# Optimization experiments

Measured on AMD Instinct MI355X. Metric: run time of the kernel, lower is better.

Reference implementation:

```python
import jax, jax.numpy as jnp
import numpy as np

T, D, H, F, A = 65536, 128, 128, 100, 18  # steps, obs_dim, gru hidden, head width, n_actions


def setup_inputs() -> dict:
    key = jax.random.key(0)
    ks = jax.random.split(key, 20)
    p = lambda k, shape, s=0.05: jax.random.normal(k, shape, dtype=jnp.float32) * s
    return {
        "obs": jax.random.normal(ks[0], (T, D), dtype=jnp.float32),
        "W1": p(ks[1], (D, H)), "b1": jnp.zeros((H,), jnp.float32),
        # GRU layer 1: gates kernel [x;h]->2H, candidate kernel [x;r*h]->H
        "Wg1": p(ks[2], (H + H, 2 * H)), "bg1": jnp.zeros((2 * H,), jnp.float32),
        "Wc1": p(ks[3], (H + H, H)), "bc1": jnp.zeros((H,), jnp.float32),
        # GRU layer 2
        "Wg2": p(ks[4], (H + H, 2 * H)), "bg2": jnp.zeros((2 * H,), jnp.float32),
        "Wc2": p(ks[5], (H + H, H)), "bc2": jnp.zeros((H,), jnp.float32),
        "W2": p(ks[6], (H, F)), "b2": jnp.zeros((F,), jnp.float32),
        "W3": p(ks[7], (H, F)), "b3": jnp.zeros((F,), jnp.float32),
        "Wp": p(ks[8], (F, A), 0.01), "bp": jnp.zeros((A,), jnp.float32),
        "Wv": p(ks[9], (F, 1)), "bv": jnp.zeros((1,), jnp.float32),
    }


def _gru_step(h, x, Wg, bg, Wc, bc):
    # TF GRUCell math: r,u = sigmoid([x;h]Wg + bg); c = tanh([x; r*h]Wc + bc)
    g = jax.nn.sigmoid(jnp.concatenate([x, h], -1) @ Wg + bg)
    r, u = jnp.split(g, 2, axis=-1)
    c = jnp.tanh(jnp.concatenate([x, r * h], -1) @ Wc + bc)
    return u * h + (1.0 - u) * c


def reference(obs, W1, b1, Wg1, bg1, Wc1, bc1, Wg2, bg2, Wc2, bc2,
              W2, b2, W3, b3, Wp, bp, Wv, bv):
    x = jax.nn.relu(obs @ W1 + b1)  # [T, H]

    def step(carry, xt):
        h1, h2 = carry
        h1 = _gru_step(h1, xt, Wg1, bg1, Wc1, bc1)
        h2 = _gru_step(h2, h1, Wg2, bg2, Wc2, bc2)
        return (h1, h2), h2

    h0 = (jnp.zeros((H,), x.dtype), jnp.zeros((H,), x.dtype))  # zero_state, batch=1
    (h1, h2), ys = jax.lax.scan(step, h0, x)  # ys: [T, H]

    pi = jax.nn.relu(ys @ W2 + b2)
    v = jax.nn.relu(ys @ W3 + b3)
    logits = pi @ Wp + bp   # [T, A]
    value = v @ Wv + bv     # [T, 1]
    return logits, value, h1, h2
```

## Files before the change

kernel.cpp:

```cpp
#include <hip/hip_runtime.h>

#define T_STEPS 65536
#define SCHUNK 128
#define NCHUNK 512
#define RING 8


typedef float f2 __attribute__((ext_vector_type(2)));
typedef float f4 __attribute__((ext_vector_type(4)));

__device__ __forceinline__ float sigmoid_f(float x) {
  float e = __expf(-x);
  return __builtin_amdgcn_rcpf(1.0f + e);
}
__device__ __forceinline__ float tanh_f(float x) {
  float e = __expf(-2.0f * x);
  return (1.0f - e) * __builtin_amdgcn_rcpf(1.0f + e);
}

__device__ __forceinline__ void bar_lds() {
  asm volatile("s_waitcnt lgkmcnt(0)\n\ts_barrier" ::: "memory");
}

__device__ __forceinline__ float rdlane(float v, int lane) {
  return __int_as_float(__builtin_amdgcn_readlane(__float_as_int(v), lane));
}

__device__ __forceinline__ void spin_rlx(int* p) {
  while (__hip_atomic_load(p, __ATOMIC_RELAXED, __HIP_MEMORY_SCOPE_AGENT) == 0)
    __builtin_amdgcn_s_sleep(8);
}
__device__ __forceinline__ void spin_acq(int* p) {
  spin_rlx(p);
  (void)__hip_atomic_load(p, __ATOMIC_ACQUIRE, __HIP_MEMORY_SCOPE_AGENT);
}
__device__ __forceinline__ void set_flag_rel(int* p) {
  __hip_atomic_store(p, 1, __ATOMIC_RELEASE, __HIP_MEMORY_SCOPE_AGENT);
}
__device__ __forceinline__ void set_flag_rlx(int* p) {
  __hip_atomic_store(p, 1, __ATOMIC_RELAXED, __HIP_MEMORY_SCOPE_AGENT);
}

__global__ __launch_bounds__(256)
void gemm_k128(const float* __restrict__ IN, const float* __restrict__ W,
               const float* __restrict__ bias, float* __restrict__ OUT,
               int N, int relu) {
  __shared__ __align__(16) float in_t[32][132];
  const int tid = threadIdx.x;
  const int ct = tid & 63;
  const int rt = tid >> 6;
  const int R0 = blockIdx.x * 32;

  const f4* src = (const f4*)(IN + (size_t)R0 * 128);
#pragma unroll
  for (int q = 0; q < 4; ++q) {
    int f4i = tid + 256 * q;
    int r = f4i >> 5, c4 = f4i & 31;
    f4 v = src[f4i];
    *(f4*)&in_t[r][c4 * 4] = v;
  }
  __syncthreads();

  f2 acc[8][4];
#pragma unroll
  for (int r = 0; r < 8; ++r)
#pragma unroll
    for (int m = 0; m < 4; ++m) acc[r][m] = (f2)0.0f;

  for (int kp = 0; kp < 64; ++kp) {
    f2 iv[8];
#pragma unroll
    for (int r = 0; r < 8; ++r)
      iv[r] = *(const f2*)&in_t[rt * 8 + r][2 * kp];
    f2 wv[4];
#pragma unroll
    for (int m = 0; m < 4; ++m) {
      int c = ct + 64 * m;
      if (c < N) {
        wv[m].x = W[(2 * kp) * N + c];
        wv[m].y = W[(2 * kp + 1) * N + c];
      } else {
        wv[m] = (f2)0.0f;
      }
    }
#pragma unroll
    for (int r = 0; r < 8; ++r)
#pragma unroll
      for (int m = 0; m < 4; ++m)
        acc[r][m] = __builtin_elementwise_fma(iv[r], wv[m], acc[r][m]);
  }

#pragma unroll
  for (int m = 0; m < 4; ++m) {
    int c = ct + 64 * m;
    if (c < N) {
      float b = bias[c];
#pragma unroll
      for (int r = 0; r < 8; ++r) {
        float v = acc[r][m].x + acc[r][m].y + b;
        if (relu) v = fmaxf(v, 0.0f);
        OUT[(size_t)(R0 + rt * 8 + r) * N + c] = v;
      }
    }
  }
}

#define GRU_STEP(LT, AR, AU, CXV)                                             \
  do {                                                                        \
    f2 ga0 = (f2)0.0f, ga1 = (f2)0.0f, ga2 = (f2)0.0f, ga3 = (f2)0.0f;        \
    _Pragma("unroll")                                                         \
    for (int qq = 0; qq < 16; ++qq) {                                         \
      f2 hp;                                                                  \
      hp.x = rdlane(hself, 2 * qq);                                           \
      hp.y = rdlane(hself, 2 * qq + 1);                                       \
      ga0 = __builtin_elementwise_fma(hp, wgt[qq][0], ga0);                   \
      ga1 = __builtin_elementwise_fma(hp, wgt[qq][1], ga1);                   \
      ga2 = __builtin_elementwise_fma(hp, wgt[qq][2], ga2);                   \
      ga3 = __builtin_elementwise_fma(hp, wgt[qq][3], ga3);                   \
    }                                                                         \
    pg[(l + 0) * 5 + w] = ga0.x + ga0.y;                                      \
    pg[(l + 64) * 5 + w] = ga1.x + ga1.y;                                     \
    pg[(l + 128) * 5 + w] = ga2.x + ga2.y;                                    \
    pg[(l + 192) * 5 + w] = ga3.x + ga3.y;                                    \
    bar_lds();                                                                \
    float rpre = ((pg[o_r * 5 + 0] + pg[o_r * 5 + 1]) +                       \
                  (pg[o_r * 5 + 2] + pg[o_r * 5 + 3])) + (AR);                \
    float upre = ((pg[o_u * 5 + 0] + pg[o_u * 5 + 1]) +                       \
                  (pg[o_u * 5 + 2] + pg[o_u * 5 + 3])) + (AU);                \
    float rg = sigmoid_f(rpre);                                               \
    float ugv = sigmoid_f(upre);                                              \
    float rhv = rg * hself;                                                   \
    f2 ca0 = (f2)0.0f, ca1 = (f2)0.0f;                                        \
    _Pragma("unroll")                                                         \
    for (int qq = 0; qq < 16; ++qq) {                                         \
      f2 rp;                                                                  \
      rp.x = rdlane(rhv, 2 * qq);                                             \
      rp.y = rdlane(rhv, 2 * qq + 1);                                         \
      ca0 = __builtin_elementwise_fma(rp, wct[qq][0], ca0);                   \
      ca1 = __builtin_elementwise_fma(rp, wct[qq][1], ca1);                   \
    }                                                                         \
    pc[(l + 0) * 5 + w] = ca0.x + ca0.y;                                      \
    pc[(l + 64) * 5 + w] = ca1.x + ca1.y;                                     \
    bar_lds();                                                                \
    float cpre = ((pc[o_r * 5 + 0] + pc[o_r * 5 + 1]) +                       \
                  (pc[o_r * 5 + 2] + pc[o_r * 5 + 3])) + (CXV);               \
    float cv = tanh_f(cpre);                                                  \
    hself = ugv * hself + (1.0f - ugv) * cv;                                  \
    if (half == 0) hc[(LT) * 128 + o_r] = hself;                              \
  } while (0)

__device__ void scan_role(const float* __restrict__ A, const float* __restrict__ CX,
                          const float* __restrict__ Wgh, const float* __restrict__ Wch,
                          float* __restrict__ hout, int hout_is_ring,
                          float* __restrict__ hfinal,
                          int* relf, int* acka, int* ackb, int* wfa, int* wfb) {
  __shared__ float pg[256 * 5];
  __shared__ float pc[128 * 5];
  const int tid = threadIdx.x;
  const int w = tid >> 6;
  const int l = tid & 63;
  const int j = l & 31;
  const int half = l >> 5;
  const int o_r = 32 * w + j;
  const int o_u = o_r + 128;

  f2 wgt[16][4];
  f2 wct[16][2];
#pragma unroll
  for (int q = 0; q < 16; ++q) {
#pragma unroll
    for (int m = 0; m < 4; ++m) {
      wgt[q][m].x = Wgh[(32 * w + 2 * q) * 256 + l + 64 * m];
      wgt[q][m].y = Wgh[(32 * w + 2 * q + 1) * 256 + l + 64 * m];
    }
#pragma unroll
    for (int n = 0; n < 2; ++n) {
      wct[q][n].x = Wch[(32 * w + 2 * q) * 128 + l + 64 * n];
      wct[q][n].y = Wch[(32 * w + 2 * q + 1) * 128 + l + 64 * n];
    }
  }

  float hself = 0.0f;

  for (int c = 0; c < NCHUNK; ++c) {
    if (wfa) { spin_acq(&wfa[c]); spin_acq(&wfb[c]); }
    if (relf && c >= RING) {
      spin_rlx(&acka[c - RING]);
      spin_rlx(&ackb[c - RING]);
    }
    const float* Ac = A + (size_t)c * SCHUNK * 256;
    const float* Cc = CX + (size_t)c * SCHUNK * 128;
    float* hc = hout_is_ring ? hout + (size_t)(c & (RING - 1)) * SCHUNK * 128
                             : hout + (size_t)c * SCHUNK * 128;

    float arc[4], auc[4], cxc[4], arn[4], aun[4], cxn[4];
#pragma unroll
    for (int q = 0; q < 4; ++q) {
      arc[q] = Ac[q * 256 + o_r];
      auc[q] = Ac[q * 256 + o_u];
      cxc[q] = Cc[q * 128 + o_r];
    }
    for (int t0 = 0; t0 < SCHUNK; t0 += 4) {
      const int nb = (t0 + 4 < SCHUNK) ? t0 + 4 : 0;
#pragma unroll
      for (int q = 0; q < 4; ++q) {
        arn[q] = Ac[(nb + q) * 256 + o_r];
        aun[q] = Ac[(nb + q) * 256 + o_u];
        cxn[q] = Cc[(nb + q) * 128 + o_r];
      }
#pragma unroll
      for (int q = 0; q < 4; ++q) {
        GRU_STEP(t0 + q, arc[q], auc[q], cxc[q]);
      }
#pragma unroll
      for (int q = 0; q < 4; ++q) { arc[q] = arn[q]; auc[q] = aun[q]; cxc[q] = cxn[q]; }
    }
    if (relf) {
      __syncthreads();
      if (tid == 0) set_flag_rel(&relf[c]);
    }
  }
  if (half == 0) hfinal[o_r] = hself;
}

__global__ void dummy_decl_anchor() {}

__device__ void gemv_gate_role(const float* __restrict__ ring,
                               const float* __restrict__ W,
                               const float* __restrict__ bias,
                               float* __restrict__ OUT,
                               int* inflag, int* ack, int* outflag) {
  __shared__ __align__(16) float hst[SCHUNK * 128];
  const int tid = threadIdx.x;
  const int l = tid & 63;
  const int col = tid;

  f2 wcol[64];
#pragma unroll
  for (int q = 0; q < 64; ++q) {
    wcol[q].x = W[(2 * q) * 256 + col];
    wcol[q].y = W[(2 * q + 1) * 256 + col];
  }
  const float bcol = bias[col];

  for (int c = 0; c < NCHUNK; ++c) {
    spin_acq(&inflag[c]);
    const f4* slot = (const f4*)(ring + (size_t)(c & (RING - 1)) * SCHUNK * 128);
    f4* hst4 = (f4*)hst;
#pragma unroll
    for (int q = 0; q < 16; ++q) hst4[tid + 256 * q] = slot[tid + 256 * q];
    __syncthreads();
    if (tid == 0) set_flag_rlx(&ack[c]);

    float* outc = OUT + (size_t)c * SCHUNK * 256;
    for (int t = 0; t < SCHUNK; ++t) {
      f2 hreg = *(const f2*)&hst[t * 128 + 2 * l];
      f2 a0 = (f2)0.0f, a1 = (f2)0.0f, a2 = (f2)0.0f, a3 = (f2)0.0f;
#pragma unroll
      for (int q = 0; q < 16; ++q) {
        f2 h0, h1, h2, h3;
        h0.x = rdlane(hreg.x, 4 * q);     h0.y = rdlane(hreg.y, 4 * q);
        h1.x = rdlane(hreg.x, 4 * q + 1); h1.y = rdlane(hreg.y, 4 * q + 1);
        h2.x = rdlane(hreg.x, 4 * q + 2); h2.y = rdlane(hreg.y, 4 * q + 2);
        h3.x = rdlane(hreg.x, 4 * q + 3); h3.y = rdlane(hreg.y, 4 * q + 3);
        a0 = __builtin_elementwise_fma(h0, wcol[4 * q], a0);
        a1 = __builtin_elementwise_fma(h1, wcol[4 * q + 1], a1);
        a2 = __builtin_elementwise_fma(h2, wcol[4 * q + 2], a2);
        a3 = __builtin_elementwise_fma(h3, wcol[4 * q + 3], a3);
      }
      f2 s = (a0 + a1) + (a2 + a3);
      outc[t * 256 + col] = s.x + s.y + bcol;
    }
    __syncthreads();
    if (tid == 0) set_flag_rel(&outflag[c]);
  }
}

__device__ void gemv_cand_role(const float* __restrict__ ring,
                               const float* __restrict__ W,
                               const float* __restrict__ bias,
                               float* __restrict__ OUT,
                               int* inflag, int* ack, int* outflag) {
  __shared__ __align__(16) float hst[SCHUNK * 128];
  const int tid = threadIdx.x;
  const int l = tid & 63;
  const int col = tid & 127;
  const int par = tid >> 7;

  f2 wcol[64];
#pragma unroll
  for (int q = 0; q < 64; ++q) {
    wcol[q].x = W[(2 * q) * 128 + col];
    wcol[q].y = W[(2 * q + 1) * 128 + col];
  }
  const float bcol = bias[col];

  for (int c = 0; c < NCHUNK; ++c) {
    spin_acq(&inflag[c]);
    const f4* slot = (const f4*)(ring + (size_t)(c & (RING - 1)) * SCHUNK * 128);
    f4* hst4 = (f4*)hst;
#pragma unroll
    for (int q = 0; q < 16; ++q) hst4[tid + 256 * q] = slot[tid + 256 * q];
    __syncthreads();
    if (tid == 0) set_flag_rlx(&ack[c]);

    float* outc = OUT + (size_t)c * SCHUNK * 128;
    for (int s = 0; s < SCHUNK / 2; ++s) {
      const int t = 2 * s + par;
      f2 hreg = *(const f2*)&hst[t * 128 + 2 * l];
      f2 a0 = (f2)0.0f, a1 = (f2)0.0f, a2 = (f2)0.0f, a3 = (f2)0.0f;
#pragma unroll
      for (int q = 0; q < 16; ++q) {
        f2 h0, h1, h2, h3;
        h0.x = rdlane(hreg.x, 4 * q);     h0.y = rdlane(hreg.y, 4 * q);
        h1.x = rdlane(hreg.x, 4 * q + 1); h1.y = rdlane(hreg.y, 4 * q + 1);
        h2.x = rdlane(hreg.x, 4 * q + 2); h2.y = rdlane(hreg.y, 4 * q + 2);
        h3.x = rdlane(hreg.x, 4 * q + 3); h3.y = rdlane(hreg.y, 4 * q + 3);
        a0 = __builtin_elementwise_fma(h0, wcol[4 * q], a0);
        a1 = __builtin_elementwise_fma(h1, wcol[4 * q + 1], a1);
        a2 = __builtin_elementwise_fma(h2, wcol[4 * q + 2], a2);
        a3 = __builtin_elementwise_fma(h3, wcol[4 * q + 3], a3);
      }
      f2 sm = (a0 + a1) + (a2 + a3);
      outc[t * 128 + col] = sm.x + sm.y + bcol;
    }
    __syncthreads();
    if (tid == 0) set_flag_rel(&outflag[c]);
  }
}

__global__ __launch_bounds__(256, 1)
void pipeline(const float* __restrict__ A1, const float* __restrict__ C1X,
              const float* __restrict__ Wg1, const float* __restrict__ Wc1,
              const float* __restrict__ Wg2, const float* __restrict__ bg2,
              const float* __restrict__ Wc2, const float* __restrict__ bc2,
              float* ring, float* A2, float* C2X, float* YS,
              float* h1f, float* h2f, int* flags) {
  int* flag1 = flags;
  int* acka  = flags + 512;
  int* ackb  = flags + 1024;
  int* f2a   = flags + 1536;
  int* f2b   = flags + 2048;
  const int role = blockIdx.x;
  if (role == 0)
    scan_role(A1, C1X, Wg1 + 128 * 256, Wc1 + 128 * 128, ring, 1, h1f,
              flag1, acka, ackb, nullptr, nullptr);
  else if (role == 1)
    gemv_gate_role(ring, Wg2, bg2, A2, flag1, acka, f2a);
  else if (role == 2)
    gemv_cand_role(ring, Wc2, bc2, C2X, flag1, ackb, f2b);
  else
    scan_role(A2, C2X, Wg2 + 128 * 256, Wc2 + 128 * 128, YS, 0, h2f,
              nullptr, nullptr, nullptr, f2a, f2b);
}

__global__ __launch_bounds__(256)
void proj_heads(const float* __restrict__ PI, const float* __restrict__ V,
                const float* __restrict__ Wp, const float* __restrict__ bp,
                const float* __restrict__ Wv, const float* __restrict__ bv,
                float* __restrict__ logits, float* __restrict__ value) {
  __shared__ float pi_t[128][101];
  __shared__ float v_t[128][101];
  __shared__ float wp_s[100][18];
  __shared__ float wv_s[100];
  __shared__ float bp_s[18];
  __shared__ float bv_s;
  const int tid = threadIdx.x;
  const int R0 = blockIdx.x * 128;

  for (int idx = tid; idx < 12800; idx += 256) {
    int r = idx / 100, c = idx - r * 100;
    pi_t[r][c] = PI[(size_t)R0 * 100 + idx];
    v_t[r][c] = V[(size_t)R0 * 100 + idx];
  }
  for (int idx = tid; idx < 1800; idx += 256) ((float*)wp_s)[idx] = Wp[idx];
  if (tid < 100) wv_s[tid] = Wv[tid];
  if (tid < 18) bp_s[tid] = bp[tid];
  if (tid == 0) bv_s = bv[0];
  __syncthreads();

  const int r = tid >> 1, h = tid & 1;
  float acc[9];
#pragma unroll
  for (int m = 0; m < 9; ++m) acc[m] = bp_s[h * 9 + m];
  float vacc = bv_s;
#pragma unroll 4
  for (int c = 0; c < 100; ++c) {
    float p = pi_t[r][c];
#pragma unroll
    for (int m = 0; m < 9; ++m) acc[m] = fmaf(p, wp_s[c][h * 9 + m], acc[m]);
    if (h) vacc = fmaf(v_t[r][c], wv_s[c], vacc);
  }
  size_t t = (size_t)R0 + r;
#pragma unroll
  for (int m = 0; m < 9; ++m) logits[t * 18 + h * 9 + m] = acc[m];
  if (h) value[t] = vacc;
}

extern "C" void kernel_launch(void* const* d_in, const int* in_sizes, int n_in,
                              void* d_out, int out_size, void* d_ws, size_t ws_size,
                              hipStream_t stream) {
  const float* obs = (const float*)d_in[0];
  const float* W1  = (const float*)d_in[1];
  const float* b1  = (const float*)d_in[2];
  const float* Wg1 = (const float*)d_in[3];
  const float* bg1 = (const float*)d_in[4];
  const float* Wc1 = (const float*)d_in[5];
  const float* bc1 = (const float*)d_in[6];
  const float* Wg2 = (const float*)d_in[7];
  const float* bg2 = (const float*)d_in[8];
  const float* Wc2 = (const float*)d_in[9];
  const float* bc2 = (const float*)d_in[10];
  const float* W2  = (const float*)d_in[11];
  const float* b2  = (const float*)d_in[12];
  const float* W3  = (const float*)d_in[13];
  const float* b3  = (const float*)d_in[14];
  const float* Wp  = (const float*)d_in[15];
  const float* bp  = (const float*)d_in[16];
  const float* Wv  = (const float*)d_in[17];
  const float* bv  = (const float*)d_in[18];

  float* out = (float*)d_out;
  float* ws  = (float*)d_ws;
  const int T = T_STEPS;

  float* A1   = ws + 0;
  float* C1X  = ws + 16777216;
  float* ring = ws + 25165824;
  int*   flags = (int*)(ws + 25296896);
  float* X    = ws + 33554432;
  float* YS   = ws + 33554432;
  float* PIb  = ws + 0;
  float* Vb   = ws + 8388608;

  float* logits = out;
  float* value  = out + (size_t)T * 18;
  float* h1f    = out + (size_t)T * 18 + T;
  float* h2f    = h1f + 128;

  dim3 b256(256);
  hipMemsetAsync(flags, 0, 2560 * sizeof(int), stream);
  gemm_k128<<<T / 32, b256, 0, stream>>>(obs, W1, b1, X, 128, 1);
  gemm_k128<<<T / 32, b256, 0, stream>>>(X, Wg1, bg1, A1, 256, 0);
  gemm_k128<<<T / 32, b256, 0, stream>>>(X, Wc1, bc1, C1X, 128, 0);
  pipeline<<<4, b256, 0, stream>>>(A1, C1X, Wg1, Wc1, Wg2, bg2, Wc2, bc2,
                                   ring, A1 , C1X , YS,
                                   h1f, h2f, flags);
  gemm_k128<<<T / 32, b256, 0, stream>>>(YS, W2, b2, PIb, 100, 1);
  gemm_k128<<<T / 32, b256, 0, stream>>>(YS, W3, b3, Vb, 100, 1);
  proj_heads<<<T / 128, b256, 0, stream>>>(PIb, Vb, Wp, bp, Wv, bv, logits, value);
}
```

Baseline: 53.06 ms.

## Double pipeline block width to 512 threads, splitting recurrent matvec across eight waves

The persistent pipeline kernel now launches with 512 threads per role block instead of 256. In the GRU scan roles, each of the eight waves handles 16 rows of the hidden-state reduction instead of 32, which halves the per-wave serial FMA/lane-read chain on the recurrence's critical path. The cost is an 8-way partial-sum reduction through LDS instead of a 4-way one. The GEMV roles split timesteps across the extra threads, and the LDS staging buffer moves into the kernel so the roles share one allocation. The risks are more barrier cost per step with eight waves and higher register pressure under the new launch bounds.

```diff
diff --git a/kernel.cpp b/kernel.cpp
--- a/kernel.cpp
+++ b/kernel.cpp
@@ -109,44 +109,50 @@
   do {                                                                        \
     f2 ga0 = (f2)0.0f, ga1 = (f2)0.0f, ga2 = (f2)0.0f, ga3 = (f2)0.0f;        \
     _Pragma("unroll")                                                         \
-    for (int qq = 0; qq < 16; ++qq) {                                         \
+    for (int m = 0; m < 8; ++m) {                                             \
       f2 hp;                                                                  \
-      hp.x = rdlane(hself, 2 * qq);                                           \
-      hp.y = rdlane(hself, 2 * qq + 1);                                       \
-      ga0 = __builtin_elementwise_fma(hp, wgt[qq][0], ga0);                   \
-      ga1 = __builtin_elementwise_fma(hp, wgt[qq][1], ga1);                   \
-      ga2 = __builtin_elementwise_fma(hp, wgt[qq][2], ga2);                   \
-      ga3 = __builtin_elementwise_fma(hp, wgt[qq][3], ga3);                   \
+      hp.x = rdlane(hself, 2 * m);                                            \
+      hp.y = rdlane(hself, 2 * m + 1);                                        \
+      ga0 = __builtin_elementwise_fma(hp, wgt[m][0], ga0);                    \
+      ga1 = __builtin_elementwise_fma(hp, wgt[m][1], ga1);                    \
+      ga2 = __builtin_elementwise_fma(hp, wgt[m][2], ga2);                    \
+      ga3 = __builtin_elementwise_fma(hp, wgt[m][3], ga3);                    \
     }                                                                         \
-    pg[(l + 0) * 5 + w] = ga0.x + ga0.y;                                      \
-    pg[(l + 64) * 5 + w] = ga1.x + ga1.y;                                     \
-    pg[(l + 128) * 5 + w] = ga2.x + ga2.y;                                    \
-    pg[(l + 192) * 5 + w] = ga3.x + ga3.y;                                    \
+    pg[(l + 0) * 9 + w] = ga0.x + ga0.y;                                      \
+    pg[(l + 64) * 9 + w] = ga1.x + ga1.y;                                     \
+    pg[(l + 128) * 9 + w] = ga2.x + ga2.y;                                    \
+    pg[(l + 192) * 9 + w] = ga3.x + ga3.y;                                    \
     bar_lds();                                                                \
-    float rpre = ((pg[o_r * 5 + 0] + pg[o_r * 5 + 1]) +                       \
-                  (pg[o_r * 5 + 2] + pg[o_r * 5 + 3])) + (AR);                \
-    float upre = ((pg[o_u * 5 + 0] + pg[o_u * 5 + 1]) +                       \
-                  (pg[o_u * 5 + 2] + pg[o_u * 5 + 3])) + (AU);                \
+    float rpre = (((pg[o_r * 9 + 0] + pg[o_r * 9 + 1]) +                      \
+                   (pg[o_r * 9 + 2] + pg[o_r * 9 + 3])) +                     \
+                  ((pg[o_r * 9 + 4] + pg[o_r * 9 + 5]) +                      \
+                   (pg[o_r * 9 + 6] + pg[o_r * 9 + 7]))) + (AR);              \
+    float upre = (((pg[o_u * 9 + 0] + pg[o_u * 9 + 1]) +                      \
+                   (pg[o_u * 9 + 2] + pg[o_u * 9 + 3])) +                     \
+                  ((pg[o_u * 9 + 4] + pg[o_u * 9 + 5]) +                      \
+                   (pg[o_u * 9 + 6] + pg[o_u * 9 + 7]))) + (AU);              \
     float rg = sigmoid_f(rpre);                                               \
     float ugv = sigmoid_f(upre);                                              \
     float rhv = rg * hself;                                                   \
     f2 ca0 = (f2)0.0f, ca1 = (f2)0.0f;                                        \
     _Pragma("unroll")                                                         \
-    for (int qq = 0; qq < 16; ++qq) {                                         \
+    for (int m = 0; m < 8; ++m) {                                             \
       f2 rp;                                                                  \
-      rp.x = rdlane(rhv, 2 * qq);                                             \
-      rp.y = rdlane(rhv, 2 * qq + 1);                                         \
-      ca0 = __builtin_elementwise_fma(rp, wct[qq][0], ca0);                   \
-      ca1 = __builtin_elementwise_fma(rp, wct[qq][1], ca1);                   \
+      rp.x = rdlane(rhv, 2 * m);                                              \
+      rp.y = rdlane(rhv, 2 * m + 1);                                          \
+      ca0 = __builtin_elementwise_fma(rp, wct[m][0], ca0);                    \
+      ca1 = __builtin_elementwise_fma(rp, wct[m][1], ca1);                    \
     }                                                                         \
-    pc[(l + 0) * 5 + w] = ca0.x + ca0.y;                                      \
-    pc[(l + 64) * 5 + w] = ca1.x + ca1.y;                                     \
+    pc[(l + 0) * 9 + w] = ca0.x + ca0.y;                                      \
+    pc[(l + 64) * 9 + w] = ca1.x + ca1.y;                                     \
     bar_lds();                                                                \
-    float cpre = ((pc[o_r * 5 + 0] + pc[o_r * 5 + 1]) +                       \
-                  (pc[o_r * 5 + 2] + pc[o_r * 5 + 3])) + (CXV);               \
+    float cpre = (((pc[o_r * 9 + 0] + pc[o_r * 9 + 1]) +                      \
+                   (pc[o_r * 9 + 2] + pc[o_r * 9 + 3])) +                     \
+                  ((pc[o_r * 9 + 4] + pc[o_r * 9 + 5]) +                      \
+                   (pc[o_r * 9 + 6] + pc[o_r * 9 + 7]))) + (CXV);             \
     float cv = tanh_f(cpre);                                                  \
     hself = ugv * hself + (1.0f - ugv) * cv;                                  \
-    if (half == 0) hc[(LT) * 128 + o_r] = hself;                              \
+    if (l < 16) hc[(LT) * 128 + o_r] = hself;                                 \
   } while (0)
 
 __device__ void scan_role(const float* __restrict__ A, const float* __restrict__ CX,
@@ -154,29 +160,28 @@
                           float* __restrict__ hout, int hout_is_ring,
                           float* __restrict__ hfinal,
                           int* relf, int* acka, int* ackb, int* wfa, int* wfb) {
-  __shared__ float pg[256 * 5];
-  __shared__ float pc[128 * 5];
+  __shared__ float pg[256 * 9];
+  __shared__ float pc[128 * 9];
   const int tid = threadIdx.x;
   const int w = tid >> 6;
   const int l = tid & 63;
-  const int j = l & 31;
-  const int half = l >> 5;
-  const int o_r = 32 * w + j;
+  const int j = l & 15;
+  const int o_r = 16 * w + j;
   const int o_u = o_r + 128;
 
-  f2 wgt[16][4];
-  f2 wct[16][2];
-#pragma unroll
-  for (int q = 0; q < 16; ++q) {
-#pragma unroll
-    for (int m = 0; m < 4; ++m) {
-      wgt[q][m].x = Wgh[(32 * w + 2 * q) * 256 + l + 64 * m];
-      wgt[q][m].y = Wgh[(32 * w + 2 * q + 1) * 256 + l + 64 * m];
-    }
-#pragma unroll
-    for (int n = 0; n < 2; ++n) {
-      wct[q][n].x = Wch[(32 * w + 2 * q) * 128 + l + 64 * n];
-      wct[q][n].y = Wch[(32 * w + 2 * q + 1) * 128 + l + 64 * n];
+  f2 wgt[8][4];
+  f2 wct[8][2];
+#pragma unroll
+  for (int m = 0; m < 8; ++m) {
+#pragma unroll
+    for (int c = 0; c < 4; ++c) {
+      wgt[m][c].x = Wgh[(16 * w + 2 * m) * 256 + l + 64 * c];
+      wgt[m][c].y = Wgh[(16 * w + 2 * m + 1) * 256 + l + 64 * c];
+    }
+#pragma unroll
+    for (int c = 0; c < 2; ++c) {
+      wct[m][c].x = Wch[(16 * w + 2 * m) * 128 + l + 64 * c];
+      wct[m][c].y = Wch[(16 * w + 2 * m + 1) * 128 + l + 64 * c];
     }
   }
 
@@ -220,20 +225,19 @@
       if (tid == 0) set_flag_rel(&relf[c]);
     }
   }
-  if (half == 0) hfinal[o_r] = hself;
-}
-
-__global__ void dummy_decl_anchor() {}
+  if (l < 16) hfinal[o_r] = hself;
+}
 
 __device__ void gemv_gate_role(const float* __restrict__ ring,
                                const float* __restrict__ W,
                                const float* __restrict__ bias,
                                float* __restrict__ OUT,
-                               int* inflag, int* ack, int* outflag) {
-  __shared__ __align__(16) float hst[SCHUNK * 128];
+                               int* inflag, int* ack, int* outflag,
+                               float* hst) {
   const int tid = threadIdx.x;
   const int l = tid & 63;
-  const int col = tid;
+  const int col = tid & 255;
+  const int par = tid >> 8;
 
   f2 wcol[64];
 #pragma unroll
@@ -248,12 +252,13 @@
     const f4* slot = (const f4*)(ring + (size_t)(c & (RING - 1)) * SCHUNK * 128);
     f4* hst4 = (f4*)hst;
 #pragma unroll
-    for (int q = 0; q < 16; ++q) hst4[tid + 256 * q] = slot[tid + 256 * q];
+    for (int q = 0; q < 8; ++q) hst4[tid + 512 * q] = slot[tid + 512 * q];
     __syncthreads();
     if (tid == 0) set_flag_rlx(&ack[c]);
 
     float* outc = OUT + (size_t)c * SCHUNK * 256;
-    for (int t = 0; t < SCHUNK; ++t) {
+    for (int s = 0; s < SCHUNK / 2; ++s) {
+      const int t = 2 * s + par;
       f2 hreg = *(const f2*)&hst[t * 128 + 2 * l];
       f2 a0 = (f2)0.0f, a1 = (f2)0.0f, a2 = (f2)0.0f, a3 = (f2)0.0f;
 #pragma unroll
@@ -268,8 +273,8 @@
         a2 = __builtin_elementwise_fma(h2, wcol[4 * q + 2], a2);
         a3 = __builtin_elementwise_fma(h3, wcol[4 * q + 3], a3);
       }
-      f2 s = (a0 + a1) + (a2 + a3);
-      outc[t * 256 + col] = s.x + s.y + bcol;
+      f2 sm = (a0 + a1) + (a2 + a3);
+      outc[t * 256 + col] = sm.x + sm.y + bcol;
     }
     __syncthreads();
     if (tid == 0) set_flag_rel(&outflag[c]);
@@ -280,8 +285,8 @@
                                const float* __restrict__ W,
                                const float* __restrict__ bias,
                                float* __restrict__ OUT,
-                               int* inflag, int* ack, int* outflag) {
-  __shared__ __align__(16) float hst[SCHUNK * 128];
+                               int* inflag, int* ack, int* outflag,
+                               float* hst) {
   const int tid = threadIdx.x;
   const int l = tid & 63;
   const int col = tid & 127;
@@ -300,13 +305,13 @@
     const f4* slot = (const f4*)(ring + (size_t)(c & (RING - 1)) * SCHUNK * 128);
     f4* hst4 = (f4*)hst;
 #pragma unroll
-    for (int q = 0; q < 16; ++q) hst4[tid + 256 * q] = slot[tid + 256 * q];
+    for (int q = 0; q < 8; ++q) hst4[tid + 512 * q] = slot[tid + 512 * q];
     __syncthreads();
     if (tid == 0) set_flag_rlx(&ack[c]);
 
     float* outc = OUT + (size_t)c * SCHUNK * 128;
-    for (int s = 0; s < SCHUNK / 2; ++s) {
-      const int t = 2 * s + par;
+    for (int s = 0; s < SCHUNK / 4; ++s) {
+      const int t = 4 * s + par;
       f2 hreg = *(const f2*)&hst[t * 128 + 2 * l];
       f2 a0 = (f2)0.0f, a1 = (f2)0.0f, a2 = (f2)0.0f, a3 = (f2)0.0f;
 #pragma unroll
@@ -329,13 +334,14 @@
   }
 }
 
-__global__ __launch_bounds__(256, 1)
+__global__ __launch_bounds__(512, 2)
 void pipeline(const float* __restrict__ A1, const float* __restrict__ C1X,
               const float* __restrict__ Wg1, const float* __restrict__ Wc1,
               const float* __restrict__ Wg2, const float* __restrict__ bg2,
               const float* __restrict__ Wc2, const float* __restrict__ bc2,
               float* ring, float* A2, float* C2X, float* YS,
               float* h1f, float* h2f, int* flags) {
+  __shared__ __align__(16) float hst[SCHUNK * 128];
   int* flag1 = flags;
   int* acka  = flags + 512;
   int* ackb  = flags + 1024;
@@ -346,9 +352,9 @@
     scan_role(A1, C1X, Wg1 + 128 * 256, Wc1 + 128 * 128, ring, 1, h1f,
               flag1, acka, ackb, nullptr, nullptr);
   else if (role == 1)
-    gemv_gate_role(ring, Wg2, bg2, A2, flag1, acka, f2a);
+    gemv_gate_role(ring, Wg2, bg2, A2, flag1, acka, f2a, hst);
   else if (role == 2)
-    gemv_cand_role(ring, Wc2, bc2, C2X, flag1, ackb, f2b);
+    gemv_cand_role(ring, Wc2, bc2, C2X, flag1, ackb, f2b, hst);
   else
     scan_role(A2, C2X, Wg2 + 128 * 256, Wc2 + 128 * 128, YS, 0, h2f,
               nullptr, nullptr, nullptr, f2a, f2b);
@@ -443,9 +449,9 @@
   gemm_k128<<<T / 32, b256, 0, stream>>>(obs, W1, b1, X, 128, 1);
   gemm_k128<<<T / 32, b256, 0, stream>>>(X, Wg1, bg1, A1, 256, 0);
   gemm_k128<<<T / 32, b256, 0, stream>>>(X, Wc1, bc1, C1X, 128, 0);
-  pipeline<<<4, b256, 0, stream>>>(A1, C1X, Wg1, Wc1, Wg2, bg2, Wc2, bc2,
-                                   ring, A1 , C1X , YS,
-                                   h1f, h2f, flags);
+  pipeline<<<4, dim3(512), 0, stream>>>(A1, C1X, Wg1, Wc1, Wg2, bg2, Wc2, bc2,
+                                        ring, A1 , C1X , YS,
+                                        h1f, h2f, flags);
   gemm_k128<<<T / 32, b256, 0, stream>>>(YS, W2, b2, PIb, 100, 1);
   gemm_k128<<<T / 32, b256, 0, stream>>>(YS, W3, b3, Vb, 100, 1);
   proj_heads<<<T / 128, b256, 0, stream>>>(PIb, Vb, Wp, bp, Wv, bv, logits, value);
```

Result: slower. 56.86 ms (+7.2%).

## Merge both GRU layer scans into one 512-thread block with a chunk lag

Applied to the files above, without the earlier changes.

Layer-1 and layer-2 recurrent scans now run as two wave groups inside a single 512-thread block, with layer 2 trailing by two chunks. Both groups share the per-step barriers, and an `act` predicate masks out the inactive group during the prologue and epilogue. The gate and candidate GEMV roles also move to 512 threads, split the timesteps across thread halves, and use one shared LDS staging buffer, so the pipeline drops from 4 blocks to 3. The aim is to use more threads per block and fewer blocks. The cost is that the two scans are coupled in lockstep and compete for the same CU's SIMDs, which may lengthen the serial critical path.

```diff
diff --git a/kernel.cpp b/kernel.cpp
--- a/kernel.cpp
+++ b/kernel.cpp
@@ -4,6 +4,7 @@
 #define SCHUNK 128
 #define NCHUNK 512
 #define RING 8
+#define LAG 2
 
 
 typedef float f2 __attribute__((ext_vector_type(2)));
@@ -107,62 +108,79 @@
 
 #define GRU_STEP(LT, AR, AU, CXV)                                             \
   do {                                                                        \
-    f2 ga0 = (f2)0.0f, ga1 = (f2)0.0f, ga2 = (f2)0.0f, ga3 = (f2)0.0f;        \
-    _Pragma("unroll")                                                         \
-    for (int qq = 0; qq < 16; ++qq) {                                         \
-      f2 hp;                                                                  \
-      hp.x = rdlane(hself, 2 * qq);                                           \
-      hp.y = rdlane(hself, 2 * qq + 1);                                       \
-      ga0 = __builtin_elementwise_fma(hp, wgt[qq][0], ga0);                   \
-      ga1 = __builtin_elementwise_fma(hp, wgt[qq][1], ga1);                   \
-      ga2 = __builtin_elementwise_fma(hp, wgt[qq][2], ga2);                   \
-      ga3 = __builtin_elementwise_fma(hp, wgt[qq][3], ga3);                   \
+    if (act) {                                                                \
+      f2 ga0 = (f2)0.0f, ga1 = (f2)0.0f, ga2 = (f2)0.0f, ga3 = (f2)0.0f;      \
+      _Pragma("unroll")                                                       \
+      for (int qq = 0; qq < 16; ++qq) {                                       \
+        f2 hp;                                                                \
+        hp.x = rdlane(hself, 2 * qq);                                         \
+        hp.y = rdlane(hself, 2 * qq + 1);                                     \
+        ga0 = __builtin_elementwise_fma(hp, wgt[qq][0], ga0);                 \
+        ga1 = __builtin_elementwise_fma(hp, wgt[qq][1], ga1);                 \
+        ga2 = __builtin_elementwise_fma(hp, wgt[qq][2], ga2);                 \
+        ga3 = __builtin_elementwise_fma(hp, wgt[qq][3], ga3);                 \
+      }                                                                       \
+      pg[(l + 0) * 5 + w] = ga0.x + ga0.y;                                    \
+      pg[(l + 64) * 5 + w] = ga1.x + ga1.y;                                   \
+      pg[(l + 128) * 5 + w] = ga2.x + ga2.y;                                  \
+      pg[(l + 192) * 5 + w] = ga3.x + ga3.y;                                  \
     }                                                                         \
-    pg[(l + 0) * 5 + w] = ga0.x + ga0.y;                                      \
-    pg[(l + 64) * 5 + w] = ga1.x + ga1.y;                                     \
-    pg[(l + 128) * 5 + w] = ga2.x + ga2.y;                                    \
-    pg[(l + 192) * 5 + w] = ga3.x + ga3.y;                                    \
     bar_lds();                                                                \
-    float rpre = ((pg[o_r * 5 + 0] + pg[o_r * 5 + 1]) +                       \
-                  (pg[o_r * 5 + 2] + pg[o_r * 5 + 3])) + (AR);                \
-    float upre = ((pg[o_u * 5 + 0] + pg[o_u * 5 + 1]) +                       \
-                  (pg[o_u * 5 + 2] + pg[o_u * 5 + 3])) + (AU);                \
-    float rg = sigmoid_f(rpre);                                               \
-    float ugv = sigmoid_f(upre);                                              \
-    float rhv = rg * hself;                                                   \
-    f2 ca0 = (f2)0.0f, ca1 = (f2)0.0f;                                        \
-    _Pragma("unroll")                                                         \
-    for (int qq = 0; qq < 16; ++qq) {                                         \
-      f2 rp;                                                                  \
-      rp.x = rdlane(rhv, 2 * qq);                                             \
-      rp.y = rdlane(rhv, 2 * qq + 1);                                         \
-      ca0 = __builtin_elementwise_fma(rp, wct[qq][0], ca0);                   \
-      ca1 = __builtin_elementwise_fma(rp, wct[qq][1], ca1);                   \
+    float rhv = 0.0f, ugv = 0.0f;                                             \
+    if (act) {                                                                \
+      float rpre = ((pg[o_r * 5 + 0] + pg[o_r * 5 + 1]) +                     \
+                    (pg[o_r * 5 + 2] + pg[o_r * 5 + 3])) + (AR);              \
+      float upre = ((pg[o_u * 5 + 0] + pg[o_u * 5 + 1]) +                     \
+                    (pg[o_u * 5 + 2] + pg[o_u * 5 + 3])) + (AU);              \
+      float rg = sigmoid_f(rpre);                                             \
+      ugv = sigmoid_f(upre);                                                  \
+      rhv = rg * hself;                                                       \
+      f2 ca0 = (f2)0.0f, ca1 = (f2)0.0f;                                      \
+      _Pragma("unroll")                                                       \
+      for (int qq = 0; qq < 16; ++qq) {                                       \
+        f2 rp;                                                                \
+        rp.x = rdlane(rhv, 2 * qq);                                           \
+        rp.y = rdlane(rhv, 2 * qq + 1);                                       \
+        ca0 = __builtin_elementwise_fma(rp, wct[qq][0], ca0);                 \
+        ca1 = __builtin_elementwise_fma(rp, wct[qq][1], ca1);                 \
+      }                                                                       \
+      pc[(l + 0) * 5 + w] = ca0.x + ca0.y;                                    \
+      pc[(l + 64) * 5 + w] = ca1.x + ca1.y;                                   \
     }                                                                         \
-    pc[(l + 0) * 5 + w] = ca0.x + ca0.y;                                      \
-    pc[(l + 64) * 5 + w] = ca1.x + ca1.y;                                     \
     bar_lds();                                                                \
-    float cpre = ((pc[o_r * 5 + 0] + pc[o_r * 5 + 1]) +                       \
-                  (pc[o_r * 5 + 2] + pc[o_r * 5 + 3])) + (CXV);               \
-    float cv = tanh_f(cpre);                                                  \
-    hself = ugv * hself + (1.0f - ugv) * cv;                                  \
-    if (half == 0) hc[(LT) * 128 + o_r] = hself;                              \
+    if (act) {                                                                \
+      float cpre = ((pc[o_r * 5 + 0] + pc[o_r * 5 + 1]) +                     \
+                    (pc[o_r * 5 + 2] + pc[o_r * 5 + 3])) + (CXV);             \
+      float cv = tanh_f(cpre);                                                \
+      hself = ugv * hself + (1.0f - ugv) * cv;                                \
+      if (half == 0) hc[(LT) * 128 + o_r] = hself;                            \
+    }                                                                         \
   } while (0)
 
-__device__ void scan_role(const float* __restrict__ A, const float* __restrict__ CX,
-                          const float* __restrict__ Wgh, const float* __restrict__ Wch,
-                          float* __restrict__ hout, int hout_is_ring,
-                          float* __restrict__ hfinal,
-                          int* relf, int* acka, int* ackb, int* wfa, int* wfb) {
-  __shared__ float pg[256 * 5];
-  __shared__ float pc[128 * 5];
+__device__ void merged_scans(const float* __restrict__ A1, const float* __restrict__ C1X,
+                             const float* __restrict__ Wg1h, const float* __restrict__ Wc1h,
+                             const float* __restrict__ Wg2h, const float* __restrict__ Wc2h,
+                             float* __restrict__ ring, const float* __restrict__ A2,
+                             const float* __restrict__ C2X, float* __restrict__ YS,
+                             float* __restrict__ h1f, float* __restrict__ h2f,
+                             int* relf, int* acka, int* ackb, int* wfa, int* wfb) {
+  __shared__ float pgs[2][256 * 5];
+  __shared__ float pcs[2][128 * 5];
   const int tid = threadIdx.x;
-  const int w = tid >> 6;
+  const int w8 = tid >> 6;
+  const int s = w8 >> 2;
+  const int w = w8 & 3;
   const int l = tid & 63;
   const int j = l & 31;
   const int half = l >> 5;
   const int o_r = 32 * w + j;
   const int o_u = o_r + 128;
+  float* pg = pgs[s];
+  float* pc = pcs[s];
+  const float* Wgh = s ? Wg2h : Wg1h;
+  const float* Wch = s ? Wc2h : Wc1h;
+  const float* Abase = s ? A2 : A1;
+  const float* Cbase = s ? C2X : C1X;
 
   f2 wgt[16][4];
   f2 wct[16][2];
@@ -182,31 +200,40 @@
 
   float hself = 0.0f;
 
-  for (int c = 0; c < NCHUNK; ++c) {
-    if (wfa) { spin_acq(&wfa[c]); spin_acq(&wfb[c]); }
-    if (relf && c >= RING) {
-      spin_rlx(&acka[c - RING]);
-      spin_rlx(&ackb[c - RING]);
-    }
-    const float* Ac = A + (size_t)c * SCHUNK * 256;
-    const float* Cc = CX + (size_t)c * SCHUNK * 128;
-    float* hc = hout_is_ring ? hout + (size_t)(c & (RING - 1)) * SCHUNK * 128
-                             : hout + (size_t)c * SCHUNK * 128;
+  for (int gc = 0; gc < NCHUNK + LAG; ++gc) {
+    const int c = s ? gc - LAG : gc;
+    const bool act = (c >= 0) && (c < NCHUNK);
+    const int cc = act ? c : 0;
+    if (act) {
+      if (s == 0) {
+        if (c >= RING) { spin_rlx(&acka[c - RING]); spin_rlx(&ackb[c - RING]); }
+      } else {
+        spin_acq(&wfa[c]); spin_acq(&wfb[c]);
+      }
+    }
+    const float* Ac = Abase + (size_t)cc * SCHUNK * 256;
+    const float* Cc = Cbase + (size_t)cc * SCHUNK * 128;
+    float* hc = s ? (YS + (size_t)cc * SCHUNK * 128)
+                  : (ring + (size_t)(cc & (RING - 1)) * SCHUNK * 128);
 
     float arc[4], auc[4], cxc[4], arn[4], aun[4], cxn[4];
-#pragma unroll
-    for (int q = 0; q < 4; ++q) {
-      arc[q] = Ac[q * 256 + o_r];
-      auc[q] = Ac[q * 256 + o_u];
-      cxc[q] = Cc[q * 128 + o_r];
+    if (act) {
+#pragma unroll
+      for (int q = 0; q < 4; ++q) {
+        arc[q] = Ac[q * 256 + o_r];
+        auc[q] = Ac[q * 256 + o_u];
+        cxc[q] = Cc[q * 128 + o_r];
+      }
     }
     for (int t0 = 0; t0 < SCHUNK; t0 += 4) {
       const int nb = (t0 + 4 < SCHUNK) ? t0 + 4 : 0;
-#pragma unroll
-      for (int q = 0; q < 4; ++q) {
-        arn[q] = Ac[(nb + q) * 256 + o_r];
-        aun[q] = Ac[(nb + q) * 256 + o_u];
-        cxn[q] = Cc[(nb + q) * 128 + o_r];
+      if (act) {
+#pragma unroll
+        for (int q = 0; q < 4; ++q) {
+          arn[q] = Ac[(nb + q) * 256 + o_r];
+          aun[q] = Ac[(nb + q) * 256 + o_u];
+          cxn[q] = Cc[(nb + q) * 128 + o_r];
+        }
       }
 #pragma unroll
       for (int q = 0; q < 4; ++q) {
@@ -215,25 +242,25 @@
 #pragma unroll
       for (int q = 0; q < 4; ++q) { arc[q] = arn[q]; auc[q] = aun[q]; cxc[q] = cxn[q]; }
     }
-    if (relf) {
-      __syncthreads();
-      if (tid == 0) set_flag_rel(&relf[c]);
-    }
-  }
-  if (half == 0) hfinal[o_r] = hself;
-}
-
-__global__ void dummy_decl_anchor() {}
+    __syncthreads();
+    if (tid == 0 && gc < NCHUNK) set_flag_rel(&relf[gc]);
+  }
+  if (half == 0) {
+    if (s == 0) h1f[o_r] = hself;
+    else        h2f[o_r] = hself;
+  }
+}
 
 __device__ void gemv_gate_role(const float* __restrict__ ring,
                                const float* __restrict__ W,
                                const float* __restrict__ bias,
                                float* __restrict__ OUT,
-                               int* inflag, int* ack, int* outflag) {
-  __shared__ __align__(16) float hst[SCHUNK * 128];
+                               int* inflag, int* ack, int* outflag,
+                               float* hst) {
   const int tid = threadIdx.x;
   const int l = tid & 63;
-  const int col = tid;
+  const int col = tid & 255;
+  const int par = tid >> 8;
 
   f2 wcol[64];
 #pragma unroll
@@ -248,12 +275,13 @@
     const f4* slot = (const f4*)(ring + (size_t)(c & (RING - 1)) * SCHUNK * 128);
     f4* hst4 = (f4*)hst;
 #pragma unroll
-    for (int q = 0; q < 16; ++q) hst4[tid + 256 * q] = slot[tid + 256 * q];
+    for (int q = 0; q < 8; ++q) hst4[tid + 512 * q] = slot[tid + 512 * q];
     __syncthreads();
     if (tid == 0) set_flag_rlx(&ack[c]);
 
     float* outc = OUT + (size_t)c * SCHUNK * 256;
-    for (int t = 0; t < SCHUNK; ++t) {
+    for (int s = 0; s < SCHUNK / 2; ++s) {
+      const int t = 2 * s + par;
       f2 hreg = *(const f2*)&hst[t * 128 + 2 * l];
       f2 a0 = (f2)0.0f, a1 = (f2)0.0f, a2 = (f2)0.0f, a3 = (f2)0.0f;
 #pragma unroll
@@ -268,8 +296,8 @@
         a2 = __builtin_elementwise_fma(h2, wcol[4 * q + 2], a2);
         a3 = __builtin_elementwise_fma(h3, wcol[4 * q + 3], a3);
       }
-      f2 s = (a0 + a1) + (a2 + a3);
-      outc[t * 256 + col] = s.x + s.y + bcol;
+      f2 sm = (a0 + a1) + (a2 + a3);
+      outc[t * 256 + col] = sm.x + sm.y + bcol;
     }
     __syncthreads();
     if (tid == 0) set_flag_rel(&outflag[c]);
@@ -280,8 +308,8 @@
                                const float* __restrict__ W,
                                const float* __restrict__ bias,
                                float* __restrict__ OUT,
-                               int* inflag, int* ack, int* outflag) {
-  __shared__ __align__(16) float hst[SCHUNK * 128];
+                               int* inflag, int* ack, int* outflag,
+                               float* hst) {
   const int tid = threadIdx.x;
   const int l = tid & 63;
   const int col = tid & 127;
@@ -300,13 +328,13 @@
     const f4* slot = (const f4*)(ring + (size_t)(c & (RING - 1)) * SCHUNK * 128);
     f4* hst4 = (f4*)hst;
 #pragma unroll
-    for (int q = 0; q < 16; ++q) hst4[tid + 256 * q] = slot[tid + 256 * q];
+    for (int q = 0; q < 8; ++q) hst4[tid + 512 * q] = slot[tid + 512 * q];
     __syncthreads();
     if (tid == 0) set_flag_rlx(&ack[c]);
 
     float* outc = OUT + (size_t)c * SCHUNK * 128;
-    for (int s = 0; s < SCHUNK / 2; ++s) {
-      const int t = 2 * s + par;
+    for (int s = 0; s < SCHUNK / 4; ++s) {
+      const int t = 4 * s + par;
       f2 hreg = *(const f2*)&hst[t * 128 + 2 * l];
       f2 a0 = (f2)0.0f, a1 = (f2)0.0f, a2 = (f2)0.0f, a3 = (f2)0.0f;
 #pragma unroll
@@ -329,13 +357,14 @@
   }
 }
 
-__global__ __launch_bounds__(256, 1)
+__global__ __launch_bounds__(512, 1)
 void pipeline(const float* __restrict__ A1, const float* __restrict__ C1X,
               const float* __restrict__ Wg1, const float* __restrict__ Wc1,
               const float* __restrict__ Wg2, const float* __restrict__ bg2,
               const float* __restrict__ Wc2, const float* __restrict__ bc2,
               float* ring, float* A2, float* C2X, float* YS,
               float* h1f, float* h2f, int* flags) {
+  __shared__ __align__(16) float hst[SCHUNK * 128];
   int* flag1 = flags;
   int* acka  = flags + 512;
   int* ackb  = flags + 1024;
@@ -343,15 +372,14 @@
   int* f2b   = flags + 2048;
   const int role = blockIdx.x;
   if (role == 0)
-    scan_role(A1, C1X, Wg1 + 128 * 256, Wc1 + 128 * 128, ring, 1, h1f,
-              flag1, acka, ackb, nullptr, nullptr);
+    merged_scans(A1, C1X, Wg1 + 128 * 256, Wc1 + 128 * 128,
+                 Wg2 + 128 * 256, Wc2 + 128 * 128,
+                 ring, A2, C2X, YS, h1f, h2f,
+                 flag1, acka, ackb, f2a, f2b);
   else if (role == 1)
-    gemv_gate_role(ring, Wg2, bg2, A2, flag1, acka, f2a);
-  else if (role == 2)
-    gemv_cand_role(ring, Wc2, bc2, C2X, flag1, ackb, f2b);
+    gemv_gate_role(ring, Wg2, bg2, A2, flag1, acka, f2a, hst);
   else
-    scan_role(A2, C2X, Wg2 + 128 * 256, Wc2 + 128 * 128, YS, 0, h2f,
-              nullptr, nullptr, nullptr, f2a, f2b);
+    gemv_cand_role(ring, Wc2, bc2, C2X, flag1, ackb, f2b, hst);
 }
 
 __global__ __launch_bounds__(256)
@@ -443,9 +471,9 @@
   gemm_k128<<<T / 32, b256, 0, stream>>>(obs, W1, b1, X, 128, 1);
   gemm_k128<<<T / 32, b256, 0, stream>>>(X, Wg1, bg1, A1, 256, 0);
   gemm_k128<<<T / 32, b256, 0, stream>>>(X, Wc1, bc1, C1X, 128, 0);
-  pipeline<<<4, b256, 0, stream>>>(A1, C1X, Wg1, Wc1, Wg2, bg2, Wc2, bc2,
-                                   ring, A1 , C1X , YS,
-                                   h1f, h2f, flags);
+  pipeline<<<3, dim3(512), 0, stream>>>(A1, C1X, Wg1, Wc1, Wg2, bg2, Wc2, bc2,
+                                        ring, A1 , C1X , YS,
+                                        h1f, h2f, flags);
   gemm_k128<<<T / 32, b256, 0, stream>>>(YS, W2, b2, PIb, 100, 1);
   gemm_k128<<<T / 32, b256, 0, stream>>>(YS, W3, b3, Vb, 100, 1);
   proj_heads<<<T / 128, b256, 0, stream>>>(PIb, Vb, Wp, bp, Wv, bv, logits, value);
```

After: 76.61 ms. +44.4%, slower.
